# Kernel optimization log

Hardware: AMD Instinct MI355X
Metric: run time of the kernel (lower is better)

The kernel has to match this reference:

```python
import jax, jax.numpy as jnp
import numpy as np

M, K, N = 64, 4096, 11008
GROUPSIZE = 64
MAXQ = 7  # 3-bit
ZERO = (MAXQ + 1) // 2  # symmetric zero point = 4


def setup_inputs() -> dict:
    key = jax.random.key(0)
    k1, k2, k3 = jax.random.split(key, 3)
    A = jax.random.normal(k1, (M, K), dtype=jnp.float32)
    # 3-bit quantized weight codes in [0, 7], logical shape (k, n)
    q = jax.random.randint(k2, (K, N), 0, MAXQ + 1, dtype=jnp.int32)
    # per-group scales, shape (k // groupsize, n); keep positive like real scales
    s = jax.random.uniform(k3, (K // GROUPSIZE, N), dtype=jnp.float32, minval=0.005, maxval=0.02)
    return {"A": A, "q": q, "s": s}


def reference(A, q, s):
    k, n = q.shape
    g = k // s.shape[0]  # groupsize (64)
    # dequantize: W[i, j] = (q[i, j] - 4) * s[i // g, j]
    centered = (q - ZERO).astype(s.dtype)              # (k, n)
    W = (centered.reshape(-1, g, n) * s[:, None, :]).reshape(k, n)
    # C = A @ W  (fused dequant-GEMM in the CUDA kernel)
    return jnp.matmul(A, W)
```

## Files before the change

### kernel.cpp

```cpp
#include <hip/hip_runtime.h>

#define K_ 4096
#define N_ 11008
#define M_ 64
#define SB 8
#define CB 86
#define BK 32
#define BN 128
#define KBAND (K_ / SB)
#define NSTEP (KBAND / BK)

typedef __attribute__((ext_vector_type(8))) short bf16x8;
typedef __attribute__((ext_vector_type(4))) float f32x4;
typedef __attribute__((ext_vector_type(4))) unsigned uint4v;
typedef __attribute__((ext_vector_type(4))) float float4v;
typedef __attribute__((ext_vector_type(4))) unsigned short ushort4v;

static __device__ __forceinline__ unsigned rne_bits(float f) {
  unsigned u = __builtin_bit_cast(unsigned, f);
  return u + 0x7fffu + ((u >> 16) & 1u);
}
static __device__ __forceinline__ unsigned pack_bf16(float lo, float hi) {
  return (rne_bits(hi) & 0xffff0000u) | (rne_bits(lo) >> 16);
}
static __device__ __forceinline__ unsigned short bf16_1(float f) {
  return (unsigned short)(rne_bits(f) >> 16);
}

__global__ __launch_bounds__(256) void cvtA_frag_kernel(
    const float* __restrict__ A, unsigned* __restrict__ Apf) {
  const int kt = blockIdx.x;
  const int mt = threadIdx.x >> 6;
  const int l  = threadIdx.x & 63;
  const int row = mt * 16 + (l & 15);
  const int kk  = kt * 32 + (l >> 4) * 8;
  const float* ap = A + (size_t)row * K_ + kk;
  uint4v b = { pack_bf16(ap[0], ap[1]), pack_bf16(ap[2], ap[3]),
               pack_bf16(ap[4], ap[5]), pack_bf16(ap[6], ap[7]) };
  *reinterpret_cast<uint4v*>(Apf + ((size_t)(kt * 4 + mt) * 64 + l) * 4) = b;
}

template <bool FROM_FRAG, bool ATOMIC>
__global__ __launch_bounds__(512, 8) void dq_gemm_kernel(
    const int* __restrict__ q, const float* __restrict__ s,
    const unsigned* __restrict__ Apf, const float* __restrict__ Af,
    unsigned short* __restrict__ P, float* __restrict__ out) {
  __shared__ int tile[2][BK * BN];

  const int tid = threadIdx.x;
  const int l   = tid & 63;
  const int w   = tid >> 6;
  const int fr  = l & 15;
  const int lg  = l >> 4;
  const int cb  = blockIdx.x % CB;
  const int sb  = blockIdx.x / CB;
  const int n0  = cb * BN;
  const int k0  = sb * KBAND;
  const int cw  = w * 16;

  f32x4 acc[4] = {f32x4{0,0,0,0}, f32x4{0,0,0,0}, f32x4{0,0,0,0}, f32x4{0,0,0,0}};

  auto stage = [&](int buf, int kst) {
    #pragma unroll
    for (int i = 0; i < 2; ++i) {
      const int rbase = w * 4 + i * 2;
      const int row   = rbase + (l >> 5);
      const int rot   = ((row >> 3) & 3) * 8;
      const int c4    = (4 * l) & 127;
      const int src   = (c4 - rot) & 127;
      const int* gp   = q + (size_t)(kst + row) * N_ + n0 + src;
      __builtin_amdgcn_global_load_lds(
          (const __attribute__((address_space(1))) unsigned*)gp,
          (__attribute__((address_space(3))) unsigned*)&tile[buf][rbase * BN],
          16, 0, 0);
    }
  };

  auto compute = [&](int buf, int kst) {
    const int g = kst >> 6;
    const float sc = s[(size_t)g * N_ + n0 + cw + fr];
    const float sn = -4.0f * sc;

    bf16x8 af[4];
    #pragma unroll
    for (int mt = 0; mt < 4; ++mt) {
      if constexpr (FROM_FRAG) {
        af[mt] = *reinterpret_cast<const bf16x8*>(
            Apf + ((size_t)((kst >> 5) * 4 + mt) * 64 + l) * 4);
      } else {
        const float* ap = Af + (size_t)(mt * 16 + fr) * K_ + kst + 8 * lg;
        float4v v0 = *reinterpret_cast<const float4v*>(ap);
        float4v v1 = *reinterpret_cast<const float4v*>(ap + 4);
        uint4v b = { pack_bf16(v0[0], v0[1]), pack_bf16(v0[2], v0[3]),
                     pack_bf16(v1[0], v1[1]), pack_bf16(v1[2], v1[3]) };
        af[mt] = __builtin_bit_cast(bf16x8, b);
      }
    }

    const int rot = 8 * lg;
    const int ci  = (cw + fr + rot) & 127;
    unsigned pk[4];
    #pragma unroll
    for (int p = 0; p < 4; ++p) {
      const int r0 = 8 * lg + 2 * p;
      const int c0 = tile[buf][r0 * BN + ci];
      const int c1 = tile[buf][(r0 + 1) * BN + ci];
      pk[p] = pack_bf16(fmaf((float)c0, sc, sn), fmaf((float)c1, sc, sn));
    }
    uint4v bv = {pk[0], pk[1], pk[2], pk[3]};
    const bf16x8 bfrag = __builtin_bit_cast(bf16x8, bv);
    #pragma unroll
    for (int mt = 0; mt < 4; ++mt)
      acc[mt] = __builtin_amdgcn_mfma_f32_16x16x32_bf16(af[mt], bfrag, acc[mt],
                                                        0, 0, 0);
  };

  stage(0, k0);
  __syncthreads();
  for (int st = 0; st < NSTEP; ++st) {
    const int kst = k0 + st * BK;
    if (st + 1 < NSTEP) stage((st + 1) & 1, kst + BK);
    compute(st & 1, kst);
    __syncthreads();
  }

  if constexpr (ATOMIC) {
    #pragma unroll
    for (int mt = 0; mt < 4; ++mt)
      #pragma unroll
      for (int j = 0; j < 4; ++j)
        atomicAdd(out + (size_t)(mt * 16 + 4 * lg + j) * N_ + n0 + cw + fr,
                  acc[mt][j]);
  } else {
    unsigned short* Pb = P + (size_t)(cb * SB + sb) * M_ * BN;
    #pragma unroll
    for (int mt = 0; mt < 4; ++mt)
      #pragma unroll
      for (int j = 0; j < 4; ++j)
        Pb[(mt * 16 + 4 * lg + j) * BN + cw + fr] = bf16_1(acc[mt][j]);
  }
}

__global__ __launch_bounds__(256) void reduce_kernel(
    const unsigned short* __restrict__ P, float* __restrict__ out) {
  const int flat = blockIdx.x * 256 + threadIdx.x;
  const int cb = flat >> 11;
  const int r  = flat & 2047;
  const int m  = r >> 5;
  const int cq = (r & 31) * 4;
  const unsigned short* p = P + ((size_t)cb * SB * M_ + m) * BN + cq;
  float s0 = 0.f, s1 = 0.f, s2 = 0.f, s3 = 0.f;
  #pragma unroll
  for (int sb = 0; sb < SB; ++sb) {
    ushort4v v = *reinterpret_cast<const ushort4v*>(p + (size_t)sb * M_ * BN);
    s0 += __builtin_bit_cast(float, (unsigned)v[0] << 16);
    s1 += __builtin_bit_cast(float, (unsigned)v[1] << 16);
    s2 += __builtin_bit_cast(float, (unsigned)v[2] << 16);
    s3 += __builtin_bit_cast(float, (unsigned)v[3] << 16);
  }
  float4v o = {s0, s1, s2, s3};
  *reinterpret_cast<float4v*>(out + (size_t)m * N_ + cb * BN + cq) = o;
}

extern "C" void kernel_launch(void* const* d_in, const int* in_sizes, int n_in,
                              void* d_out, int out_size, void* d_ws, size_t ws_size,
                              hipStream_t stream) {
  const float* A = (const float*)d_in[0];
  const int*   q = (const int*)d_in[1];
  const float* s = (const float*)d_in[2];
  float* out = (float*)d_out;

  const size_t apBytes = (size_t)128 * 4 * 64 * 16;
  const size_t pBytes  = (size_t)CB * SB * M_ * BN * sizeof(unsigned short);
  const size_t needFull = apBytes + pBytes;

  if (ws_size >= needFull) {
    unsigned* Apf = (unsigned*)d_ws;
    unsigned short* P = (unsigned short*)((char*)d_ws + apBytes);
    hipLaunchKernelGGL(cvtA_frag_kernel, dim3(128), dim3(256), 0, stream,
                       A, Apf);
    hipLaunchKernelGGL((dq_gemm_kernel<true, false>), dim3(CB * SB), dim3(512),
                       0, stream, q, s, Apf, A, P, out);
    hipLaunchKernelGGL(reduce_kernel, dim3(688), dim3(256), 0, stream, P, out);
  } else if (ws_size >= apBytes) {
    unsigned* Apf = (unsigned*)d_ws;
    hipMemsetAsync(d_out, 0, (size_t)M_ * N_ * sizeof(float), stream);
    hipLaunchKernelGGL(cvtA_frag_kernel, dim3(128), dim3(256), 0, stream,
                       A, Apf);
    hipLaunchKernelGGL((dq_gemm_kernel<true, true>), dim3(CB * SB), dim3(512),
                       0, stream, q, s, Apf, A, (unsigned short*)nullptr, out);
  } else {
    hipMemsetAsync(d_out, 0, (size_t)M_ * N_ * sizeof(float), stream);
    hipLaunchKernelGGL((dq_gemm_kernel<false, true>), dim3(CB * SB), dim3(512),
                       0, stream, q, s, (const unsigned*)nullptr, A,
                       (unsigned short*)nullptr, out);
  }
}
```

Before: 45.05 us.

## Widen GEMM column tile to 256 and deepen split-K to 16 bands

Each wave now computes two 16-column tiles, so every A fragment feeds twice as many MFMAs. The K dimension is split into 16 bands instead of 8 to keep the block count the same. The staging, compute, store and reduce index math are all adjusted for the 256-wide tile and the 16 partial slices. In exchange, the double-buffered LDS tile grows to 64KB per block, which lowers how many blocks fit per CU, and the reduce kernel now sums 16 partials per output instead of 8.

```diff
diff --git a/kernel.cpp b/kernel.cpp
--- a/kernel.cpp
+++ b/kernel.cpp
@@ -3,10 +3,10 @@
 #define K_ 4096
 #define N_ 11008
 #define M_ 64
-#define SB 8
-#define CB 86
+#define SB 16
+#define CB 43
 #define BK 32
-#define BN 128
+#define BN 256
 #define KBAND (K_ / SB)
 #define NSTEP (KBAND / BK)
 
@@ -41,7 +41,7 @@
 }
 
 template <bool FROM_FRAG, bool ATOMIC>
-__global__ __launch_bounds__(512, 8) void dq_gemm_kernel(
+__global__ __launch_bounds__(512, 4) void dq_gemm_kernel(
     const int* __restrict__ q, const float* __restrict__ s,
     const unsigned* __restrict__ Apf, const float* __restrict__ Af,
     unsigned short* __restrict__ P, float* __restrict__ out) {
@@ -56,30 +56,33 @@
   const int sb  = blockIdx.x / CB;
   const int n0  = cb * BN;
   const int k0  = sb * KBAND;
-  const int cw  = w * 16;
-
-  f32x4 acc[4] = {f32x4{0,0,0,0}, f32x4{0,0,0,0}, f32x4{0,0,0,0}, f32x4{0,0,0,0}};
+  const int cw  = w * 32;
+
+  f32x4 acc[4][2];
+  #pragma unroll
+  for (int mt = 0; mt < 4; ++mt)
+    #pragma unroll
+    for (int nt = 0; nt < 2; ++nt)
+      acc[mt][nt] = f32x4{0.f, 0.f, 0.f, 0.f};
 
   auto stage = [&](int buf, int kst) {
     #pragma unroll
-    for (int i = 0; i < 2; ++i) {
-      const int rbase = w * 4 + i * 2;
-      const int row   = rbase + (l >> 5);
-      const int rot   = ((row >> 3) & 3) * 8;
-      const int c4    = (4 * l) & 127;
-      const int src   = (c4 - rot) & 127;
-      const int* gp   = q + (size_t)(kst + row) * N_ + n0 + src;
+    for (int i = 0; i < 4; ++i) {
+      const int row = w * 4 + i;
+      const int rot = 8 * (row >> 3);
+      const int src = (4 * l - rot) & (BN - 1);
+      const int* gp = q + (size_t)(kst + row) * N_ + n0 + src;
       __builtin_amdgcn_global_load_lds(
           (const __attribute__((address_space(1))) unsigned*)gp,
-          (__attribute__((address_space(3))) unsigned*)&tile[buf][rbase * BN],
+          (__attribute__((address_space(3))) unsigned*)&tile[buf][row * BN],
           16, 0, 0);
     }
   };
 
   auto compute = [&](int buf, int kst) {
     const int g = kst >> 6;
-    const float sc = s[(size_t)g * N_ + n0 + cw + fr];
-    const float sn = -4.0f * sc;
+    const float sc0 = s[(size_t)g * N_ + n0 + cw + fr];
+    const float sc1 = s[(size_t)g * N_ + n0 + cw + 16 + fr];
 
     bf16x8 af[4];
     #pragma unroll
@@ -98,21 +101,26 @@
     }
 
     const int rot = 8 * lg;
-    const int ci  = (cw + fr + rot) & 127;
-    unsigned pk[4];
-    #pragma unroll
-    for (int p = 0; p < 4; ++p) {
-      const int r0 = 8 * lg + 2 * p;
-      const int c0 = tile[buf][r0 * BN + ci];
-      const int c1 = tile[buf][(r0 + 1) * BN + ci];
-      pk[p] = pack_bf16(fmaf((float)c0, sc, sn), fmaf((float)c1, sc, sn));
+    #pragma unroll
+    for (int nt = 0; nt < 2; ++nt) {
+      const float sc = nt ? sc1 : sc0;
+      const float sn = -4.0f * sc;
+      const int ci = (cw + nt * 16 + fr + rot) & (BN - 1);
+      unsigned pk[4];
+      #pragma unroll
+      for (int p = 0; p < 4; ++p) {
+        const int r0 = 8 * lg + 2 * p;
+        const int c0 = tile[buf][r0 * BN + ci];
+        const int c1 = tile[buf][(r0 + 1) * BN + ci];
+        pk[p] = pack_bf16(fmaf((float)c0, sc, sn), fmaf((float)c1, sc, sn));
+      }
+      uint4v bv = {pk[0], pk[1], pk[2], pk[3]};
+      const bf16x8 bfrag = __builtin_bit_cast(bf16x8, bv);
+      #pragma unroll
+      for (int mt = 0; mt < 4; ++mt)
+        acc[mt][nt] = __builtin_amdgcn_mfma_f32_16x16x32_bf16(
+            af[mt], bfrag, acc[mt][nt], 0, 0, 0);
     }
-    uint4v bv = {pk[0], pk[1], pk[2], pk[3]};
-    const bf16x8 bfrag = __builtin_bit_cast(bf16x8, bv);
-    #pragma unroll
-    for (int mt = 0; mt < 4; ++mt)
-      acc[mt] = __builtin_amdgcn_mfma_f32_16x16x32_bf16(af[mt], bfrag, acc[mt],
-                                                        0, 0, 0);
   };
 
   stage(0, k0);
@@ -128,27 +136,33 @@
     #pragma unroll
     for (int mt = 0; mt < 4; ++mt)
       #pragma unroll
-      for (int j = 0; j < 4; ++j)
-        atomicAdd(out + (size_t)(mt * 16 + 4 * lg + j) * N_ + n0 + cw + fr,
-                  acc[mt][j]);
+      for (int nt = 0; nt < 2; ++nt)
+        #pragma unroll
+        for (int j = 0; j < 4; ++j)
+          atomicAdd(out + (size_t)(mt * 16 + 4 * lg + j) * N_ + n0 + cw +
+                        nt * 16 + fr,
+                    acc[mt][nt][j]);
   } else {
     unsigned short* Pb = P + (size_t)(cb * SB + sb) * M_ * BN;
     #pragma unroll
     for (int mt = 0; mt < 4; ++mt)
       #pragma unroll
-      for (int j = 0; j < 4; ++j)
-        Pb[(mt * 16 + 4 * lg + j) * BN + cw + fr] = bf16_1(acc[mt][j]);
+      for (int nt = 0; nt < 2; ++nt)
+        #pragma unroll
+        for (int j = 0; j < 4; ++j)
+          Pb[(mt * 16 + 4 * lg + j) * BN + cw + nt * 16 + fr] =
+              bf16_1(acc[mt][nt][j]);
   }
 }
 
 __global__ __launch_bounds__(256) void reduce_kernel(
     const unsigned short* __restrict__ P, float* __restrict__ out) {
   const int flat = blockIdx.x * 256 + threadIdx.x;
-  const int cb = flat >> 11;
-  const int r  = flat & 2047;
-  const int m  = r >> 5;
-  const int cq = (r & 31) * 4;
-  const unsigned short* p = P + ((size_t)cb * SB * M_ + m) * BN + cq;
+  const int cb = flat >> 12;
+  const int r  = flat & 4095;
+  const int m  = r >> 6;
+  const int cq = (r & 63) * 4;
+  const unsigned short* p = P + ((size_t)cb * SB + 0) * M_ * BN + m * BN + cq;
   float s0 = 0.f, s1 = 0.f, s2 = 0.f, s3 = 0.f;
   #pragma unroll
   for (int sb = 0; sb < SB; ++sb) {
```

Result: slower. 47.57 us (+5.6%).

## Deepen GEMM pipeline to four LDS buffers with async A-fragment staging

Applied to the files above, without the earlier changes.

Replaces the double-buffered main GEMM with a four-buffer pipeline that keeps three stages of q tiles in flight. The pre-converted bf16 A fragments are now staged into LDS with async global_load_lds instead of being read directly from global memory. Per-group scales are preloaded into registers, and one barrier with a manual vmcnt wait replaces the two syncthreads per step. The larger LDS footprint lowers occupancy (launch bounds 4 instead of 8), and the hand-set vmcnt counts must match the number of outstanding loads for correctness.

```diff
diff --git a/kernel.cpp b/kernel.cpp
--- a/kernel.cpp
+++ b/kernel.cpp
@@ -9,6 +9,7 @@
 #define BN 128
 #define KBAND (K_ / SB)
 #define NSTEP (KBAND / BK)
+#define NBUF 4
 
 typedef __attribute__((ext_vector_type(8))) short bf16x8;
 typedef __attribute__((ext_vector_type(4))) float f32x4;
@@ -40,11 +41,132 @@
   *reinterpret_cast<uint4v*>(Apf + ((size_t)(kt * 4 + mt) * 64 + l) * 4) = b;
 }
 
-template <bool FROM_FRAG, bool ATOMIC>
-__global__ __launch_bounds__(512, 8) void dq_gemm_kernel(
+__global__ __launch_bounds__(512, 4) void dq_gemm_pipe(
     const int* __restrict__ q, const float* __restrict__ s,
-    const unsigned* __restrict__ Apf, const float* __restrict__ Af,
-    unsigned short* __restrict__ P, float* __restrict__ out) {
+    const unsigned* __restrict__ Apf, unsigned short* __restrict__ P) {
+  __shared__ int qtile[NBUF][BK * BN];
+  __shared__ int atile[NBUF][1024];
+
+  const int tid = threadIdx.x;
+  const int l   = tid & 63;
+  const int w   = tid >> 6;
+  const int fr  = l & 15;
+  const int lg  = l >> 4;
+  const int cb  = blockIdx.x % CB;
+  const int sb  = blockIdx.x / CB;
+  const int n0  = cb * BN;
+  const int k0  = sb * KBAND;
+  const int cw  = w * 16;
+
+  float scv[NSTEP / 2];
+  #pragma unroll
+  for (int g = 0; g < NSTEP / 2; ++g)
+    scv[g] = s[(size_t)((k0 >> 6) + g) * N_ + n0 + cw + fr];
+
+  f32x4 acc[4] = {f32x4{0,0,0,0}, f32x4{0,0,0,0}, f32x4{0,0,0,0}, f32x4{0,0,0,0}};
+
+  auto stage = [&](int buf, int kst) {
+    #pragma unroll
+    for (int i = 0; i < 2; ++i) {
+      const int rbase = w * 4 + i * 2;
+      const int row   = rbase + (l >> 5);
+      const int rot   = ((row >> 3) & 3) * 8;
+      const int c4    = (4 * l) & 127;
+      const int src   = (c4 - rot) & 127;
+      const int* gp   = q + (size_t)(kst + row) * N_ + n0 + src;
+      __builtin_amdgcn_global_load_lds(
+          (const __attribute__((address_space(1))) unsigned*)gp,
+          (__attribute__((address_space(3))) unsigned*)&qtile[buf][rbase * BN],
+          16, 0, 0);
+    }
+    const unsigned* ab = Apf + (size_t)(kst >> 5) * 1024 + w * 128;
+    #pragma unroll
+    for (int i = 0; i < 2; ++i) {
+      __builtin_amdgcn_global_load_lds(
+          (const __attribute__((address_space(1))) unsigned*)(ab + i * 64 + l),
+          (__attribute__((address_space(3))) unsigned*)&atile[buf][w * 128 + i * 64],
+          4, 0, 0);
+    }
+  };
+
+  auto compute = [&](int buf, float sc) {
+    bf16x8 af[4];
+    #pragma unroll
+    for (int mt = 0; mt < 4; ++mt)
+      af[mt] = *reinterpret_cast<const bf16x8*>(&atile[buf][mt * 256 + l * 4]);
+    const float sn = -4.0f * sc;
+    const int rot = 8 * lg;
+    const int ci  = (cw + fr + rot) & 127;
+    unsigned pk[4];
+    #pragma unroll
+    for (int p = 0; p < 4; ++p) {
+      const int r0 = 8 * lg + 2 * p;
+      const int c0 = qtile[buf][r0 * BN + ci];
+      const int c1 = qtile[buf][(r0 + 1) * BN + ci];
+      pk[p] = pack_bf16(fmaf((float)c0, sc, sn), fmaf((float)c1, sc, sn));
+    }
+    uint4v bv = {pk[0], pk[1], pk[2], pk[3]};
+    const bf16x8 bfrag = __builtin_bit_cast(bf16x8, bv);
+    #pragma unroll
+    for (int mt = 0; mt < 4; ++mt)
+      acc[mt] = __builtin_amdgcn_mfma_f32_16x16x32_bf16(af[mt], bfrag, acc[mt],
+                                                        0, 0, 0);
+  };
+
+  stage(0, k0);
+  stage(1, k0 + BK);
+  stage(2, k0 + 2 * BK);
+
+  #pragma unroll
+  for (int st = 0; st < NSTEP - 2; ++st) {
+    asm volatile("s_waitcnt vmcnt(8)" ::: "memory");
+    __builtin_amdgcn_s_barrier();
+    __builtin_amdgcn_sched_barrier(0);
+    compute(st & 3, scv[st >> 1]);
+    if (st + 3 < NSTEP) stage((st + 3) & 3, k0 + (st + 3) * BK);
+  }
+  asm volatile("s_waitcnt vmcnt(4)" ::: "memory");
+  __builtin_amdgcn_s_barrier();
+  __builtin_amdgcn_sched_barrier(0);
+  compute((NSTEP - 2) & 3, scv[(NSTEP - 2) >> 1]);
+
+  asm volatile("s_waitcnt vmcnt(0)" ::: "memory");
+  __builtin_amdgcn_s_barrier();
+  __builtin_amdgcn_sched_barrier(0);
+  compute((NSTEP - 1) & 3, scv[(NSTEP - 1) >> 1]);
+
+  unsigned short* Pb = P + (size_t)(cb * SB + sb) * M_ * BN;
+  #pragma unroll
+  for (int mt = 0; mt < 4; ++mt)
+    #pragma unroll
+    for (int j = 0; j < 4; ++j)
+      Pb[(mt * 16 + 4 * lg + j) * BN + cw + fr] = bf16_1(acc[mt][j]);
+}
+
+__global__ __launch_bounds__(256) void reduce_kernel(
+    const unsigned short* __restrict__ P, float* __restrict__ out) {
+  const int flat = blockIdx.x * 256 + threadIdx.x;
+  const int cb = flat >> 11;
+  const int r  = flat & 2047;
+  const int m  = r >> 5;
+  const int cq = (r & 31) * 4;
+  const unsigned short* p = P + ((size_t)cb * SB * M_ + m) * BN + cq;
+  float s0 = 0.f, s1 = 0.f, s2 = 0.f, s3 = 0.f;
+  #pragma unroll
+  for (int sb = 0; sb < SB; ++sb) {
+    ushort4v v = *reinterpret_cast<const ushort4v*>(p + (size_t)sb * M_ * BN);
+    s0 += __builtin_bit_cast(float, (unsigned)v[0] << 16);
+    s1 += __builtin_bit_cast(float, (unsigned)v[1] << 16);
+    s2 += __builtin_bit_cast(float, (unsigned)v[2] << 16);
+    s3 += __builtin_bit_cast(float, (unsigned)v[3] << 16);
+  }
+  float4v o = {s0, s1, s2, s3};
+  *reinterpret_cast<float4v*>(out + (size_t)m * N_ + cb * BN + cq) = o;
+}
+
+__global__ __launch_bounds__(512, 8) void dq_gemm_basic(
+    const int* __restrict__ q, const float* __restrict__ s,
+    const float* __restrict__ Af, float* __restrict__ out) {
   __shared__ int tile[2][BK * BN];
 
   const int tid = threadIdx.x;
@@ -77,26 +199,18 @@
   };
 
   auto compute = [&](int buf, int kst) {
-    const int g = kst >> 6;
-    const float sc = s[(size_t)g * N_ + n0 + cw + fr];
+    const float sc = s[(size_t)(kst >> 6) * N_ + n0 + cw + fr];
+    bf16x8 af[4];
+    #pragma unroll
+    for (int mt = 0; mt < 4; ++mt) {
+      const float* ap = Af + (size_t)(mt * 16 + fr) * K_ + kst + 8 * lg;
+      float4v v0 = *reinterpret_cast<const float4v*>(ap);
+      float4v v1 = *reinterpret_cast<const float4v*>(ap + 4);
+      uint4v b = { pack_bf16(v0[0], v0[1]), pack_bf16(v0[2], v0[3]),
+                   pack_bf16(v1[0], v1[1]), pack_bf16(v1[2], v1[3]) };
+      af[mt] = __builtin_bit_cast(bf16x8, b);
+    }
     const float sn = -4.0f * sc;
-
-    bf16x8 af[4];
-    #pragma unroll
-    for (int mt = 0; mt < 4; ++mt) {
-      if constexpr (FROM_FRAG) {
-        af[mt] = *reinterpret_cast<const bf16x8*>(
-            Apf + ((size_t)((kst >> 5) * 4 + mt) * 64 + l) * 4);
-      } else {
-        const float* ap = Af + (size_t)(mt * 16 + fr) * K_ + kst + 8 * lg;
-        float4v v0 = *reinterpret_cast<const float4v*>(ap);
-        float4v v1 = *reinterpret_cast<const float4v*>(ap + 4);
-        uint4v b = { pack_bf16(v0[0], v0[1]), pack_bf16(v0[2], v0[3]),
-                     pack_bf16(v1[0], v1[1]), pack_bf16(v1[2], v1[3]) };
-        af[mt] = __builtin_bit_cast(bf16x8, b);
-      }
-    }
-
     const int rot = 8 * lg;
     const int ci  = (cw + fr + rot) & 127;
     unsigned pk[4];
@@ -124,42 +238,12 @@
     __syncthreads();
   }
 
-  if constexpr (ATOMIC) {
-    #pragma unroll
-    for (int mt = 0; mt < 4; ++mt)
-      #pragma unroll
-      for (int j = 0; j < 4; ++j)
-        atomicAdd(out + (size_t)(mt * 16 + 4 * lg + j) * N_ + n0 + cw + fr,
-                  acc[mt][j]);
-  } else {
-    unsigned short* Pb = P + (size_t)(cb * SB + sb) * M_ * BN;
-    #pragma unroll
-    for (int mt = 0; mt < 4; ++mt)
-      #pragma unroll
-      for (int j = 0; j < 4; ++j)
-        Pb[(mt * 16 + 4 * lg + j) * BN + cw + fr] = bf16_1(acc[mt][j]);
-  }
-}
-
-__global__ __launch_bounds__(256) void reduce_kernel(
-    const unsigned short* __restrict__ P, float* __restrict__ out) {
-  const int flat = blockIdx.x * 256 + threadIdx.x;
-  const int cb = flat >> 11;
-  const int r  = flat & 2047;
-  const int m  = r >> 5;
-  const int cq = (r & 31) * 4;
-  const unsigned short* p = P + ((size_t)cb * SB * M_ + m) * BN + cq;
-  float s0 = 0.f, s1 = 0.f, s2 = 0.f, s3 = 0.f;
-  #pragma unroll
-  for (int sb = 0; sb < SB; ++sb) {
-    ushort4v v = *reinterpret_cast<const ushort4v*>(p + (size_t)sb * M_ * BN);
-    s0 += __builtin_bit_cast(float, (unsigned)v[0] << 16);
-    s1 += __builtin_bit_cast(float, (unsigned)v[1] << 16);
-    s2 += __builtin_bit_cast(float, (unsigned)v[2] << 16);
-    s3 += __builtin_bit_cast(float, (unsigned)v[3] << 16);
-  }
-  float4v o = {s0, s1, s2, s3};
-  *reinterpret_cast<float4v*>(out + (size_t)m * N_ + cb * BN + cq) = o;
+  #pragma unroll
+  for (int mt = 0; mt < 4; ++mt)
+    #pragma unroll
+    for (int j = 0; j < 4; ++j)
+      atomicAdd(out + (size_t)(mt * 16 + 4 * lg + j) * N_ + n0 + cw + fr,
+                acc[mt][j]);
 }
 
 extern "C" void kernel_launch(void* const* d_in, const int* in_sizes, int n_in,
@@ -170,7 +254,7 @@
   const float* s = (const float*)d_in[2];
   float* out = (float*)d_out;
 
-  const size_t apBytes = (size_t)128 * 4 * 64 * 16;
+  const size_t apBytes = (size_t)128 * 1024 * sizeof(unsigned);
   const size_t pBytes  = (size_t)CB * SB * M_ * BN * sizeof(unsigned short);
   const size_t needFull = apBytes + pBytes;
 
@@ -179,20 +263,12 @@
     unsigned short* P = (unsigned short*)((char*)d_ws + apBytes);
     hipLaunchKernelGGL(cvtA_frag_kernel, dim3(128), dim3(256), 0, stream,
                        A, Apf);
-    hipLaunchKernelGGL((dq_gemm_kernel<true, false>), dim3(CB * SB), dim3(512),
-                       0, stream, q, s, Apf, A, P, out);
+    hipLaunchKernelGGL(dq_gemm_pipe, dim3(CB * SB), dim3(512), 0, stream,
+                       q, s, Apf, P);
     hipLaunchKernelGGL(reduce_kernel, dim3(688), dim3(256), 0, stream, P, out);
-  } else if (ws_size >= apBytes) {
-    unsigned* Apf = (unsigned*)d_ws;
-    hipMemsetAsync(d_out, 0, (size_t)M_ * N_ * sizeof(float), stream);
-    hipLaunchKernelGGL(cvtA_frag_kernel, dim3(128), dim3(256), 0, stream,
-                       A, Apf);
-    hipLaunchKernelGGL((dq_gemm_kernel<true, true>), dim3(CB * SB), dim3(512),
-                       0, stream, q, s, Apf, A, (unsigned short*)nullptr, out);
   } else {
     hipMemsetAsync(d_out, 0, (size_t)M_ * N_ * sizeof(float), stream);
-    hipLaunchKernelGGL((dq_gemm_kernel<false, true>), dim3(CB * SB), dim3(512),
-                       0, stream, q, s, (const unsigned*)nullptr, A,
-                       (unsigned short*)nullptr, out);
-  }
-}
+    hipLaunchKernelGGL(dq_gemm_basic, dim3(CB * SB), dim3(512), 0, stream,
+                       q, s, A, out);
+  }
+}
```

Result: faster. 44.09 us (-2.1%).
